# Kernel optimization log

Hardware: AMD Instinct MI355X
Metric: run time of the kernel (lower is better)

## Reference

```python
import jax, jax.numpy as jnp
import numpy as np

BS, SEQ, IN_DIM, EMB = 64, 1024, 512, 1024
HID = EMB // 2  # MLP hidden = embed_dim//2 = 512
RATIO = 0.3
K = max(1, int((SEQ - 2) * RATIO))  # 306
MASK_VALUE = -10000.0
BN_EPS = 1e-5


def setup_inputs() -> dict:
    key = jax.random.key(0)
    ks = jax.random.split(key, 12)
    features = jax.random.normal(ks[0], (BS, SEQ, IN_DIM), dtype=jnp.float32)
    atten = jax.random.normal(ks[1], (BS, SEQ, SEQ), dtype=jnp.float32)
    # variable-length token ids, pad_id = 0
    lengths = jax.random.randint(ks[2], (BS,), K + 14, SEQ + 1)
    tokens = jax.random.randint(ks[3], (BS, SEQ), 1, 30000)
    text = jnp.where(jnp.arange(SEQ)[None, :] < lengths[:, None], tokens, 0).astype(jnp.int64)
    s = 0.02
    lin_w = jax.random.normal(ks[4], (IN_DIM, EMB), dtype=jnp.float32) * s
    lin_b = jnp.zeros((EMB,), dtype=jnp.float32)
    w1 = jax.random.normal(ks[5], (IN_DIM, HID), dtype=jnp.float32) * s
    b1 = jnp.zeros((HID,), dtype=jnp.float32)
    g1 = jnp.ones((HID,), dtype=jnp.float32)
    be1 = jnp.zeros((HID,), dtype=jnp.float32)
    w2 = jax.random.normal(ks[6], (HID, EMB), dtype=jnp.float32) * s
    b2 = jnp.zeros((EMB,), dtype=jnp.float32)
    return {"features": features, "atten": atten, "text": text,
            "lin_w": lin_w, "lin_b": lin_b, "w1": w1, "b1": b1,
            "g1": g1, "be1": be1, "w2": w2, "b2": b2}


def _forward(features, atten, text, lin_w, lin_b, w1, b1, g1, be1, w2, b2):
    bs, seq_len, _ = atten.shape
    atten = jnp.nan_to_num(atten, nan=0.0, posinf=0.0, neginf=0.0)
    mask = (text != 0).astype(jnp.float32)                       # (bs, seq)
    token_lens = jnp.maximum(jnp.sum(text != 0, axis=1), 1)       # (bs,)
    eos_pos = jnp.clip(token_lens - 1, 0, seq_len - 1)            # (bs,)
    # mask column 0 and column eos_pos (per batch) across all rows
    col = jnp.arange(seq_len)[None, :]
    col_mask = (col == 0) | (col == eos_pos[:, None])             # (bs, seq)
    atten = jnp.where(col_mask[:, None, :], MASK_VALUE, atten)
    # masked_fill where token is pad (columns)
    atten = jnp.where(mask[:, None, :] == 0, MASK_VALUE, atten)
    atten = jax.nn.softmax(atten, axis=1)                         # softmax over rows (dim=1)
    # select the eos row per batch, weight by mask
    atten_sel = jnp.take_along_axis(atten, eos_pos[:, None, None], axis=1)[:, 0, :] * mask
    _, topk_idx = jax.lax.top_k(atten_sel, K)                     # (bs, K)
    feats_k = jnp.take_along_axis(features, topk_idx[:, :, None], axis=1)  # (bs, K, D)
    norm = jnp.maximum(jnp.linalg.norm(feats_k, axis=-1, keepdims=True), 1e-6)
    feats_k = feats_k / norm
    cap_emb = feats_k @ lin_w + lin_b                             # (bs, K, EMB)
    # MLP: Linear -> BatchNorm1d(train-mode batch stats) -> ReLU -> Linear
    xf = feats_k.reshape(bs * K, -1)
    h = xf @ w1 + b1                                              # (bs*K, HID)
    mu = jnp.mean(h, axis=0)
    var = jnp.mean((h - mu) ** 2, axis=0)                         # biased var
    h = (h - mu) / jnp.sqrt(var + BN_EPS) * g1 + be1
    h = jax.nn.relu(h)
    feats_mlp = (h @ w2 + b2).reshape(bs, K, -1)
    fused = cap_emb + feats_mlp                                   # (bs, K, EMB)
    # variable-length top-1 pooling: max over first pool_lens[b] tokens
    pool_lens = jnp.clip(token_lens - 2, 1, K)
    valid = jnp.arange(K)[None, :] < pool_lens[:, None]           # (bs, K)
    out = jnp.max(jnp.where(valid[:, :, None], fused, -jnp.inf), axis=1)
    return out.astype(jnp.float32)


def reference(features, atten, text, lin_w, lin_b, w1, b1, g1, be1, w2, b2):
    return _forward(features, atten, text, lin_w, lin_b, w1, b1, g1, be1, w2, b2)
```

## Files before the change

### kernel.cpp

```cpp
#include <hip/hip_runtime.h>
#include <cstdint>
#include <cstddef>
#include <cmath>

#define BS 64
#define SEQ 1024
#define IN_DIM 512
#define EMB 1024
#define HID 512
#define KSEL 306
#define MROWS (BS * KSEL)

typedef __bf16 bf16_t;
typedef bf16_t bf16x8 __attribute__((ext_vector_type(8)));
typedef bf16_t bf16x4 __attribute__((ext_vector_type(4)));
typedef float f32x4 __attribute__((ext_vector_type(4)));

__device__ __forceinline__ void async16(const void* g, void* l) {
  __builtin_amdgcn_global_load_lds(
      (const __attribute__((address_space(1))) unsigned int*)g,
      (__attribute__((address_space(3))) unsigned int*)l, 16, 0, 0);
}

__device__ __forceinline__ void atomicMaxF(float* a, float v) {
  if (v >= 0.f)
    atomicMax((int*)a, __float_as_int(v));
  else
    atomicMin((unsigned int*)a, __float_as_uint(v));
}

__global__ void k_meta(const int* __restrict__ text, int* __restrict__ eos,
                       float* __restrict__ out) {
  int b = blockIdx.x;
  __shared__ int cnt;
  if (threadIdx.x == 0) cnt = 0;
  __syncthreads();
  int local = 0;
  for (int i = threadIdx.x; i < SEQ; i += blockDim.x)
    local += (text[b * SEQ + i] != 0) ? 1 : 0;
  atomicAdd(&cnt, local);
  for (int c = threadIdx.x; c < EMB; c += blockDim.x)
    out[(b << 10) + c] = -INFINITY;
  __syncthreads();
  if (threadIdx.x == 0) {
    int L = cnt > 1 ? cnt : 1;
    int e = L - 1;
    if (e > SEQ - 1) e = SEQ - 1;
    eos[b] = e;
  }
}

__global__ void k_colsum(const float* __restrict__ atten, float* __restrict__ part) {
  int b = blockIdx.x;
  int r0 = blockIdx.y << 6;
  int c = threadIdx.x << 2;
  const float* base = atten + ((size_t)b << 20) + ((size_t)r0 << 10) + c;
  float4 s = {0.f, 0.f, 0.f, 0.f};
#pragma unroll 4
  for (int r = 0; r < 64; ++r) {
    float4 x = *(const float4*)(base + ((size_t)r << 10));
    s.x += __expf((isfinite(x.x) ? x.x : 0.f) - 12.f);
    s.y += __expf((isfinite(x.y) ? x.y : 0.f) - 12.f);
    s.z += __expf((isfinite(x.z) ? x.z : 0.f) - 12.f);
    s.w += __expf((isfinite(x.w) ? x.w : 0.f) - 12.f);
  }
  *(float4*)&part[((((size_t)blockIdx.y << 6) | b) << 10) | c] = s;
}

__global__ void k_selval(const float* __restrict__ atten, const int* __restrict__ text,
                         const int* __restrict__ eos, const float* __restrict__ part,
                         float* __restrict__ selval) {
  int b = blockIdx.x >> 2;
  int c = ((blockIdx.x & 3) << 8) | threadIdx.x;
  int e = eos[b];
  float cs = 0.f;
#pragma unroll
  for (int p = 0; p < 16; ++p) cs += part[(((p << 6) | b) << 10) | c];
  float v = atten[((size_t)b << 20) + ((size_t)e << 10) + c];
  if (!isfinite(v)) v = 0.f;
  int tok = text[(b << 10) | c];
  float res;
  if (tok == 0) res = 0.f;
  else if (c == 0 || c == e) res = 1.f / 1024.f;
  else res = __expf(v - 12.f) / cs;
  selval[(b << 10) | c] = res;
}

__global__ void k_topk(const float* __restrict__ selval, int* __restrict__ selidx) {
  int b = blockIdx.x;
  int i = (blockIdx.y << 8) | threadIdx.x;
  __shared__ float vals[SEQ];
  for (int j = threadIdx.x; j < SEQ; j += 256) vals[j] = selval[(b << 10) + j];
  __syncthreads();
  float vc = vals[i];
  int rank = 0;
  for (int j = 0; j < SEQ; ++j) {
    float vj = vals[j];
    rank += (vj > vc || (vj == vc && j < i)) ? 1 : 0;
  }
  if (rank < KSEL) selidx[b * KSEL + rank] = i;
}

__global__ void k_gather(const float* __restrict__ features, const int* __restrict__ sel,
                         bf16_t* __restrict__ xcat) {
  int row = blockIdx.x;
  int b = row / KSEL;
  int k = row - b * KSEL;
  int idx = sel[b * KSEL + k];
  const float4* src = (const float4*)(features + (((size_t)b << 10) + idx) * IN_DIM);
  float4 v = src[threadIdx.x];
  float ss = v.x * v.x + v.y * v.y + v.z * v.z + v.w * v.w;
#pragma unroll
  for (int off = 32; off > 0; off >>= 1) ss += __shfl_down(ss, off, 64);
  __shared__ float wsum[2];
  int lane = threadIdx.x & 63, wid = threadIdx.x >> 6;
  if (lane == 0) wsum[wid] = ss;
  __syncthreads();
  float total = wsum[0] + wsum[1];
  float scale = 1.f / fmaxf(sqrtf(total), 1e-6f);
  bf16x4 o;
  o[0] = (bf16_t)(v.x * scale);
  o[1] = (bf16_t)(v.y * scale);
  o[2] = (bf16_t)(v.z * scale);
  o[3] = (bf16_t)(v.w * scale);
  *(bf16x4*)(xcat + (size_t)row * EMB + (threadIdx.x << 2)) = o;
}

__global__ void k_transpose_bf16(const float* __restrict__ src, int srcld,
                                 bf16_t* __restrict__ dst, int dstld) {
  __shared__ float tile[32][33];
  int k0 = blockIdx.x << 5, n0 = blockIdx.y << 5;
  int tx = threadIdx.x, ty = threadIdx.y;
#pragma unroll
  for (int i = 0; i < 4; i++)
    tile[ty + 8 * i][tx] = src[(size_t)(k0 + ty + 8 * i) * srcld + n0 + tx];
  __syncthreads();
#pragma unroll
  for (int i = 0; i < 4; i++)
    dst[(size_t)(n0 + ty + 8 * i) * dstld + k0 + tx] = (bf16_t)tile[tx][ty + 8 * i];
}

template <int MODE>
__global__ __launch_bounds__(256, 2) void k_mfma_gemm(
    const bf16_t* __restrict__ A, int lda, const bf16_t* __restrict__ Bt, int ldb,
    const float* __restrict__ bias, bf16_t* __restrict__ C, int ldc, int K,
    float* __restrict__ stats, float* __restrict__ outmax) {
  __shared__ __align__(16) bf16_t As[128 * 32];
  __shared__ __align__(16) bf16_t Bs[128 * 32];
  int tid = threadIdx.x;

  int MT = gridDim.x, NT = gridDim.y;
  int nwg = MT * NT;
  int flat = blockIdx.y * MT + blockIdx.x;
  int q = nwg >> 3, r = nwg & 7;
  int xcd = flat & 7, ii = flat >> 3;
  int lin = (xcd < r ? xcd * (q + 1) : r * (q + 1) + (xcd - r) * q) + ii;
  int mtile = lin / NT;
  int ntile = lin - mtile * NT;
  int m0 = mtile << 7, n0 = ntile << 7;

  int wave = tid >> 6, lane = tid & 63;
  int wm = (wave >> 1) << 6, wn = (wave & 1) << 6;
  int lrow = lane & 15, quad = lane >> 4;

  f32x4 acc[4][4];
#pragma unroll
  for (int i = 0; i < 4; i++)
#pragma unroll
    for (int j = 0; j < 4; j++) acc[i][j] = (f32x4){0.f, 0.f, 0.f, 0.f};

  int c0 = tid, c1 = 256 + tid;
  int ar0 = c0 >> 2, ak0 = (c0 & 3) << 3;
  int ar1 = c1 >> 2, ak1 = (c1 & 3) << 3;
  const bf16_t* Ap0 = A + (size_t)(m0 + ar0) * lda + ak0;
  const bf16_t* Ap1 = A + (size_t)(m0 + ar1) * lda + ak1;
  const bf16_t* Bp0 = Bt + (size_t)(n0 + ar0) * ldb + ak0;
  const bf16_t* Bp1 = Bt + (size_t)(n0 + ar1) * ldb + ak1;

  for (int k0 = 0; k0 < K; k0 += 32) {
    async16(Ap0 + k0, &As[c0 << 3]);
    async16(Ap1 + k0, &As[c1 << 3]);
    async16(Bp0 + k0, &Bs[c0 << 3]);
    async16(Bp1 + k0, &Bs[c1 << 3]);
    __syncthreads();

    bf16x8 af[4], bfr[4];
#pragma unroll
    for (int i = 0; i < 4; i++)
      af[i] = *(const bf16x8*)&As[((wm + (i << 4) + lrow) << 5) + (quad << 3)];
#pragma unroll
    for (int j = 0; j < 4; j++)
      bfr[j] = *(const bf16x8*)&Bs[((wn + (j << 4) + lrow) << 5) + (quad << 3)];
#pragma unroll
    for (int i = 0; i < 4; i++)
#pragma unroll
      for (int j = 0; j < 4; j++)
        acc[i][j] = __builtin_amdgcn_mfma_f32_16x16x32_bf16(af[i], bfr[j], acc[i][j], 0, 0, 0);
    __syncthreads();
  }

  if (MODE == 0) {
#pragma unroll
    for (int j = 0; j < 4; j++) {
      int n = n0 + wn + (j << 4) + lrow;
      float bv = bias[n];
      float s = 0.f, qq = 0.f;
#pragma unroll
      for (int i = 0; i < 4; i++) {
        int mbase = m0 + wm + (i << 4) + (quad << 2);
#pragma unroll
        for (int rr = 0; rr < 4; rr++) {
          float v = acc[i][j][rr] + bv;
          C[(size_t)(mbase + rr) * ldc + n] = (bf16_t)v;
          s += v;
          qq += v * v;
        }
      }
      s += __shfl_xor(s, 16, 64);
      s += __shfl_xor(s, 32, 64);
      qq += __shfl_xor(qq, 16, 64);
      qq += __shfl_xor(qq, 32, 64);
      if (quad == 0) {
        atomicAdd(&stats[n], s);
        atomicAdd(&stats[HID + n], qq);
      }
    }
  } else {
    int mw = m0 + wm;
    int b0w = mw / KSEL;
    int cut = (b0w + 1) * KSEL;
#pragma unroll
    for (int j = 0; j < 4; j++) {
      int n = n0 + wn + (j << 4) + lrow;
      float bv = bias[n];
      float mx0 = -INFINITY, mx1 = -INFINITY;
#pragma unroll
      for (int i = 0; i < 4; i++) {
#pragma unroll
        for (int rr = 0; rr < 4; rr++) {
          int m = mw + (i << 4) + (quad << 2) + rr;
          float v = acc[i][j][rr] + bv;
          if (m < cut) mx0 = fmaxf(mx0, v);
          else mx1 = fmaxf(mx1, v);
        }
      }
      mx0 = fmaxf(mx0, __shfl_xor(mx0, 16, 64));
      mx0 = fmaxf(mx0, __shfl_xor(mx0, 32, 64));
      mx1 = fmaxf(mx1, __shfl_xor(mx1, 16, 64));
      mx1 = fmaxf(mx1, __shfl_xor(mx1, 32, 64));
      if (quad == 0) {
        atomicMaxF(&outmax[(b0w << 10) + n], mx0);
        if (cut < mw + 64) atomicMaxF(&outmax[((b0w + 1) << 10) + n], mx1);
      }
    }
  }
}

__global__ void k_bnparam(const float* __restrict__ stats, const float* __restrict__ g,
                          const float* __restrict__ be, float* __restrict__ scsh,
                          const float* __restrict__ lin_b, const float* __restrict__ b2,
                          float* __restrict__ biasC) {
  int c = threadIdx.x;
  biasC[c] = lin_b[c] + b2[c];
  if (c < HID) {
    float inv = 1.f / (float)MROWS;
    float mu = stats[c] * inv;
    float var = stats[HID + c] * inv - mu * mu;
    var = fmaxf(var, 0.f);
    float sc = g[c] * rsqrtf(var + 1e-5f);
    scsh[c] = sc;
    scsh[HID + c] = fmaf(-mu, sc, be[c]);
  }
}

__global__ void k_bnapply(const bf16_t* __restrict__ h, const float* __restrict__ scsh,
                          bf16_t* __restrict__ xcat) {
  size_t idx = (size_t)blockIdx.x * blockDim.x + threadIdx.x;
  bf16x8 x = ((const bf16x8*)h)[idx];
  int c = (int)(idx & 63) << 3;
  size_t row = idx >> 6;
  bf16x8 o;
#pragma unroll
  for (int t = 0; t < 8; ++t) {
    float v = (float)x[t];
    float a = fmaxf(fmaf(v, scsh[c + t], scsh[HID + c + t]), 0.f);
    o[t] = (bf16_t)a;
  }
  *(bf16x8*)(xcat + row * EMB + 512 + c) = o;
}

extern "C" void kernel_launch(void* const* d_in, const int* in_sizes, int n_in,
                              void* d_out, int out_size, void* d_ws, size_t ws_size,
                              hipStream_t stream) {
  const float* features = (const float*)d_in[0];
  const float* atten    = (const float*)d_in[1];
  const int*   text     = (const int*)d_in[2];
  const float* lin_w    = (const float*)d_in[3];
  const float* lin_b    = (const float*)d_in[4];
  const float* w1       = (const float*)d_in[5];
  const float* b1       = (const float*)d_in[6];
  const float* g1       = (const float*)d_in[7];
  const float* be1      = (const float*)d_in[8];
  const float* w2       = (const float*)d_in[9];
  const float* b2       = (const float*)d_in[10];
  float* out = (float*)d_out;

  char* ws = (char*)d_ws;
  int*    eos    = (int*)(ws + 0);
  float*  stats  = (float*)(ws + 256);
  float*  scsh   = (float*)(ws + 4608);
  float*  biasC  = (float*)(ws + 8704);
  float*  part   = (float*)(ws + 12800);
  float*  selval = (float*)(ws + 4207104UL);
  int*    selidx = (int*)(ws + 4469248UL);
  bf16_t* w1t    = (bf16_t*)(ws + 4547584UL);
  bf16_t* wcatt  = (bf16_t*)(ws + 5071872UL);
  bf16_t* xcat   = (bf16_t*)(ws + 7169024UL);
  bf16_t* h      = (bf16_t*)(ws + 47277056UL);

  hipMemsetAsync(stats, 0, 4096, stream);

  k_meta<<<BS, 256, 0, stream>>>(text, eos, out);
  k_colsum<<<dim3(BS, 16), 256, 0, stream>>>(atten, part);
  k_selval<<<BS * 4, 256, 0, stream>>>(atten, text, eos, part, selval);
  k_topk<<<dim3(BS, 4), 256, 0, stream>>>(selval, selidx);
  k_gather<<<MROWS, 128, 0, stream>>>(features, selidx, xcat);

  k_transpose_bf16<<<dim3(16, 16), dim3(32, 8), 0, stream>>>(w1, HID, w1t, IN_DIM);
  k_transpose_bf16<<<dim3(16, 32), dim3(32, 8), 0, stream>>>(lin_w, EMB, wcatt, EMB);
  k_transpose_bf16<<<dim3(16, 32), dim3(32, 8), 0, stream>>>(w2, EMB, wcatt + 512, EMB);

  k_mfma_gemm<0><<<dim3(MROWS / 128, HID / 128), 256, 0, stream>>>(
      xcat, EMB, w1t, IN_DIM, b1, h, HID, IN_DIM, stats, nullptr);

  k_bnparam<<<1, EMB, 0, stream>>>(stats, g1, be1, scsh, lin_b, b2, biasC);
  k_bnapply<<<(MROWS * (HID / 8)) / 256, 256, 0, stream>>>(h, scsh, xcat);

  k_mfma_gemm<1><<<dim3(MROWS / 128, EMB / 128), 256, 0, stream>>>(
      xcat, EMB, wcatt, EMB, biasC, nullptr, 0, EMB, nullptr, out);
}
```

Measured before the change: 577.2 us.

## Fuse GEMM1 with BatchNorm via cooperative grid sync; merge selval/topk and transposes

Replaces the GEMM1 → bnparam → bnapply sequence with a single cooperative kernel. Each block computes a 128x512 tile, holds it in registers, accumulates batch statistics with atomics, waits on a grid-wide sync, then applies BN and ReLU and writes straight into xcat. This removes the intermediate h buffer round trip and two launches. It also folds selval into the top-k kernel and merges the three weight transposes into one launch. In exchange it needs all 153 blocks of 512 threads resident at once, uses large register tiles (acc[4][8]), and the selval work is repeated for each of the 4 blockIdx.y slices.

```diff
diff --git a/kernel.cpp b/kernel.cpp
--- a/kernel.cpp
+++ b/kernel.cpp
@@ -1,7 +1,10 @@
 #include <hip/hip_runtime.h>
+#include <hip/hip_cooperative_groups.h>
 #include <cstdint>
 #include <cstddef>
 #include <cmath>
+
+namespace cg = cooperative_groups;
 
 #define BS 64
 #define SEQ 1024
@@ -67,31 +70,27 @@
   *(float4*)&part[((((size_t)blockIdx.y << 6) | b) << 10) | c] = s;
 }
 
-__global__ void k_selval(const float* __restrict__ atten, const int* __restrict__ text,
-                         const int* __restrict__ eos, const float* __restrict__ part,
-                         float* __restrict__ selval) {
-  int b = blockIdx.x >> 2;
-  int c = ((blockIdx.x & 3) << 8) | threadIdx.x;
+__global__ void k_topk(const float* __restrict__ atten, const int* __restrict__ text,
+                       const int* __restrict__ eos, const float* __restrict__ part,
+                       int* __restrict__ selidx) {
+  int b = blockIdx.x;
+  __shared__ float vals[SEQ];
   int e = eos[b];
-  float cs = 0.f;
-#pragma unroll
-  for (int p = 0; p < 16; ++p) cs += part[(((p << 6) | b) << 10) | c];
-  float v = atten[((size_t)b << 20) + ((size_t)e << 10) + c];
-  if (!isfinite(v)) v = 0.f;
-  int tok = text[(b << 10) | c];
-  float res;
-  if (tok == 0) res = 0.f;
-  else if (c == 0 || c == e) res = 1.f / 1024.f;
-  else res = __expf(v - 12.f) / cs;
-  selval[(b << 10) | c] = res;
-}
-
-__global__ void k_topk(const float* __restrict__ selval, int* __restrict__ selidx) {
-  int b = blockIdx.x;
+  for (int c = threadIdx.x; c < SEQ; c += 256) {
+    float cs = 0.f;
+#pragma unroll
+    for (int p = 0; p < 16; ++p) cs += part[(((p << 6) | b) << 10) | c];
+    float v = atten[((size_t)b << 20) + ((size_t)e << 10) + c];
+    if (!isfinite(v)) v = 0.f;
+    int tok = text[(b << 10) | c];
+    float res;
+    if (tok == 0) res = 0.f;
+    else if (c == 0 || c == e) res = 1.f / 1024.f;
+    else res = __expf(v - 12.f) / cs;
+    vals[c] = res;
+  }
+  __syncthreads();
   int i = (blockIdx.y << 8) | threadIdx.x;
-  __shared__ float vals[SEQ];
-  for (int j = threadIdx.x; j < SEQ; j += 256) vals[j] = selval[(b << 10) + j];
-  __syncthreads();
   float vc = vals[i];
   int rank = 0;
   for (int j = 0; j < SEQ; ++j) {
@@ -126,10 +125,16 @@
   *(bf16x4*)(xcat + (size_t)row * EMB + (threadIdx.x << 2)) = o;
 }
 
-__global__ void k_transpose_bf16(const float* __restrict__ src, int srcld,
-                                 bf16_t* __restrict__ dst, int dstld) {
+__global__ void k_transpose_all(const float* __restrict__ w1, const float* __restrict__ lin_w,
+                                const float* __restrict__ w2, bf16_t* __restrict__ w1t,
+                                bf16_t* __restrict__ wcatt) {
   __shared__ float tile[32][33];
-  int k0 = blockIdx.x << 5, n0 = blockIdx.y << 5;
+  int by = blockIdx.y;
+  const float* src; int srcld; bf16_t* dst; int dstld; int n0;
+  if (by < 16)      { src = w1;    srcld = HID; dst = w1t;         dstld = IN_DIM; n0 = by << 5; }
+  else if (by < 48) { src = lin_w; srcld = EMB; dst = wcatt;       dstld = EMB;    n0 = (by - 16) << 5; }
+  else              { src = w2;    srcld = EMB; dst = wcatt + 512; dstld = EMB;    n0 = (by - 48) << 5; }
+  int k0 = blockIdx.x << 5;
   int tx = threadIdx.x, ty = threadIdx.y;
 #pragma unroll
   for (int i = 0; i < 4; i++)
@@ -140,11 +145,109 @@
     dst[(size_t)(n0 + ty + 8 * i) * dstld + k0 + tx] = (bf16_t)tile[tx][ty + 8 * i];
 }
 
-template <int MODE>
-__global__ __launch_bounds__(256, 2) void k_mfma_gemm(
-    const bf16_t* __restrict__ A, int lda, const bf16_t* __restrict__ Bt, int ldb,
-    const float* __restrict__ bias, bf16_t* __restrict__ C, int ldc, int K,
-    float* __restrict__ stats, float* __restrict__ outmax) {
+__global__ __launch_bounds__(512, 1) void k_gemm1_coop(
+    const bf16_t* A,
+    const bf16_t* __restrict__ Bt,
+    const float* __restrict__ b1, const float* __restrict__ g1,
+    const float* __restrict__ be1, float* stats,
+    bf16_t* xcat_out) {
+  __shared__ __align__(16) bf16_t As[128 * 32];
+  __shared__ __align__(16) bf16_t Bs[512 * 32];
+  int tid = threadIdx.x;
+  int m0 = blockIdx.x << 7;
+  int wave = tid >> 6, lane = tid & 63;
+  int wm = (wave >> 2) << 6;
+  int wn = (wave & 3) << 7;
+  int lrow = lane & 15, quad = lane >> 4;
+
+  f32x4 acc[4][8];
+#pragma unroll
+  for (int i = 0; i < 4; i++)
+#pragma unroll
+    for (int j = 0; j < 8; j++) acc[i][j] = (f32x4){0.f, 0.f, 0.f, 0.f};
+
+  int arow = tid >> 2, ak = (tid & 3) << 3;
+  const bf16_t* Ap = A + (size_t)(m0 + arow) * EMB + ak;
+  int brow0 = tid >> 2, bk = (tid & 3) << 3;
+  const bf16_t* Bp0 = Bt + (size_t)(brow0 + 0) * IN_DIM + bk;
+  const bf16_t* Bp1 = Bt + (size_t)(brow0 + 128) * IN_DIM + bk;
+  const bf16_t* Bp2 = Bt + (size_t)(brow0 + 256) * IN_DIM + bk;
+  const bf16_t* Bp3 = Bt + (size_t)(brow0 + 384) * IN_DIM + bk;
+
+  for (int k0 = 0; k0 < IN_DIM; k0 += 32) {
+    async16(Ap + k0, &As[tid << 3]);
+    async16(Bp0 + k0, &Bs[(tid + 0) << 3]);
+    async16(Bp1 + k0, &Bs[(tid + 512) << 3]);
+    async16(Bp2 + k0, &Bs[(tid + 1024) << 3]);
+    async16(Bp3 + k0, &Bs[(tid + 1536) << 3]);
+    __syncthreads();
+
+    bf16x8 af[4], bfr[8];
+#pragma unroll
+    for (int i = 0; i < 4; i++)
+      af[i] = *(const bf16x8*)&As[((wm + (i << 4) + lrow) << 5) + (quad << 3)];
+#pragma unroll
+    for (int j = 0; j < 8; j++)
+      bfr[j] = *(const bf16x8*)&Bs[((wn + (j << 4) + lrow) << 5) + (quad << 3)];
+#pragma unroll
+    for (int i = 0; i < 4; i++)
+#pragma unroll
+      for (int j = 0; j < 8; j++)
+        acc[i][j] = __builtin_amdgcn_mfma_f32_16x16x32_bf16(af[i], bfr[j], acc[i][j], 0, 0, 0);
+    __syncthreads();
+  }
+
+#pragma unroll
+  for (int j = 0; j < 8; j++) {
+    int n = wn + (j << 4) + lrow;
+    float bv = b1[n];
+    float s = 0.f, qq = 0.f;
+#pragma unroll
+    for (int i = 0; i < 4; i++) {
+#pragma unroll
+      for (int rr = 0; rr < 4; rr++) {
+        float v = acc[i][j][rr] + bv;
+        acc[i][j][rr] = v;
+        s += v;
+        qq += v * v;
+      }
+    }
+    s += __shfl_xor(s, 16, 64);
+    s += __shfl_xor(s, 32, 64);
+    qq += __shfl_xor(qq, 16, 64);
+    qq += __shfl_xor(qq, 32, 64);
+    if (quad == 0) {
+      atomicAdd(&stats[n], s);
+      atomicAdd(&stats[HID + n], qq);
+    }
+  }
+
+  cg::this_grid().sync();
+
+  const float inv = 1.f / (float)MROWS;
+#pragma unroll
+  for (int j = 0; j < 8; j++) {
+    int n = wn + (j << 4) + lrow;
+    float mu = stats[n] * inv;
+    float var = fmaxf(stats[HID + n] * inv - mu * mu, 0.f);
+    float sc = g1[n] * rsqrtf(var + 1e-5f);
+    float sh = fmaf(-mu, sc, be1[n]);
+#pragma unroll
+    for (int i = 0; i < 4; i++) {
+      int mbase = m0 + wm + (i << 4) + (quad << 2);
+#pragma unroll
+      for (int rr = 0; rr < 4; rr++) {
+        float a = fmaxf(fmaf(acc[i][j][rr], sc, sh), 0.f);
+        xcat_out[(size_t)(mbase + rr) * EMB + 512 + n] = (bf16_t)a;
+      }
+    }
+  }
+}
+
+__global__ __launch_bounds__(256, 2) void k_gemm2(
+    const bf16_t* __restrict__ A, const bf16_t* __restrict__ Bt,
+    const float* __restrict__ lin_b, const float* __restrict__ b2,
+    float* __restrict__ outmax) {
   __shared__ __align__(16) bf16_t As[128 * 32];
   __shared__ __align__(16) bf16_t Bs[128 * 32];
   int tid = threadIdx.x;
@@ -172,12 +275,12 @@
   int c0 = tid, c1 = 256 + tid;
   int ar0 = c0 >> 2, ak0 = (c0 & 3) << 3;
   int ar1 = c1 >> 2, ak1 = (c1 & 3) << 3;
-  const bf16_t* Ap0 = A + (size_t)(m0 + ar0) * lda + ak0;
-  const bf16_t* Ap1 = A + (size_t)(m0 + ar1) * lda + ak1;
-  const bf16_t* Bp0 = Bt + (size_t)(n0 + ar0) * ldb + ak0;
-  const bf16_t* Bp1 = Bt + (size_t)(n0 + ar1) * ldb + ak1;
-
-  for (int k0 = 0; k0 < K; k0 += 32) {
+  const bf16_t* Ap0 = A + (size_t)(m0 + ar0) * EMB + ak0;
+  const bf16_t* Ap1 = A + (size_t)(m0 + ar1) * EMB + ak1;
+  const bf16_t* Bp0 = Bt + (size_t)(n0 + ar0) * EMB + ak0;
+  const bf16_t* Bp1 = Bt + (size_t)(n0 + ar1) * EMB + ak1;
+
+  for (int k0 = 0; k0 < EMB; k0 += 32) {
     async16(Ap0 + k0, &As[c0 << 3]);
     async16(Ap1 + k0, &As[c1 << 3]);
     async16(Bp0 + k0, &Bs[c0 << 3]);
@@ -199,94 +302,33 @@
     __syncthreads();
   }
 
-  if (MODE == 0) {
-#pragma unroll
-    for (int j = 0; j < 4; j++) {
-      int n = n0 + wn + (j << 4) + lrow;
-      float bv = bias[n];
-      float s = 0.f, qq = 0.f;
-#pragma unroll
-      for (int i = 0; i < 4; i++) {
-        int mbase = m0 + wm + (i << 4) + (quad << 2);
-#pragma unroll
-        for (int rr = 0; rr < 4; rr++) {
-          float v = acc[i][j][rr] + bv;
-          C[(size_t)(mbase + rr) * ldc + n] = (bf16_t)v;
-          s += v;
-          qq += v * v;
-        }
+  int mw = m0 + wm;
+  int b0w = mw / KSEL;
+  int cut = (b0w + 1) * KSEL;
+#pragma unroll
+  for (int j = 0; j < 4; j++) {
+    int n = n0 + wn + (j << 4) + lrow;
+    float bv = lin_b[n] + b2[n];
+    float mx0 = -INFINITY, mx1 = -INFINITY;
+#pragma unroll
+    for (int i = 0; i < 4; i++) {
+#pragma unroll
+      for (int rr = 0; rr < 4; rr++) {
+        int m = mw + (i << 4) + (quad << 2) + rr;
+        float v = acc[i][j][rr] + bv;
+        if (m < cut) mx0 = fmaxf(mx0, v);
+        else mx1 = fmaxf(mx1, v);
       }
-      s += __shfl_xor(s, 16, 64);
-      s += __shfl_xor(s, 32, 64);
-      qq += __shfl_xor(qq, 16, 64);
-      qq += __shfl_xor(qq, 32, 64);
-      if (quad == 0) {
-        atomicAdd(&stats[n], s);
-        atomicAdd(&stats[HID + n], qq);
-      }
-    }
-  } else {
-    int mw = m0 + wm;
-    int b0w = mw / KSEL;
-    int cut = (b0w + 1) * KSEL;
-#pragma unroll
-    for (int j = 0; j < 4; j++) {
-      int n = n0 + wn + (j << 4) + lrow;
-      float bv = bias[n];
-      float mx0 = -INFINITY, mx1 = -INFINITY;
-#pragma unroll
-      for (int i = 0; i < 4; i++) {
-#pragma unroll
-        for (int rr = 0; rr < 4; rr++) {
-          int m = mw + (i << 4) + (quad << 2) + rr;
-          float v = acc[i][j][rr] + bv;
-          if (m < cut) mx0 = fmaxf(mx0, v);
-          else mx1 = fmaxf(mx1, v);
-        }
-      }
-      mx0 = fmaxf(mx0, __shfl_xor(mx0, 16, 64));
-      mx0 = fmaxf(mx0, __shfl_xor(mx0, 32, 64));
-      mx1 = fmaxf(mx1, __shfl_xor(mx1, 16, 64));
-      mx1 = fmaxf(mx1, __shfl_xor(mx1, 32, 64));
-      if (quad == 0) {
-        atomicMaxF(&outmax[(b0w << 10) + n], mx0);
-        if (cut < mw + 64) atomicMaxF(&outmax[((b0w + 1) << 10) + n], mx1);
-      }
-    }
-  }
-}
-
-__global__ void k_bnparam(const float* __restrict__ stats, const float* __restrict__ g,
-                          const float* __restrict__ be, float* __restrict__ scsh,
-                          const float* __restrict__ lin_b, const float* __restrict__ b2,
-                          float* __restrict__ biasC) {
-  int c = threadIdx.x;
-  biasC[c] = lin_b[c] + b2[c];
-  if (c < HID) {
-    float inv = 1.f / (float)MROWS;
-    float mu = stats[c] * inv;
-    float var = stats[HID + c] * inv - mu * mu;
-    var = fmaxf(var, 0.f);
-    float sc = g[c] * rsqrtf(var + 1e-5f);
-    scsh[c] = sc;
-    scsh[HID + c] = fmaf(-mu, sc, be[c]);
-  }
-}
-
-__global__ void k_bnapply(const bf16_t* __restrict__ h, const float* __restrict__ scsh,
-                          bf16_t* __restrict__ xcat) {
-  size_t idx = (size_t)blockIdx.x * blockDim.x + threadIdx.x;
-  bf16x8 x = ((const bf16x8*)h)[idx];
-  int c = (int)(idx & 63) << 3;
-  size_t row = idx >> 6;
-  bf16x8 o;
-#pragma unroll
-  for (int t = 0; t < 8; ++t) {
-    float v = (float)x[t];
-    float a = fmaxf(fmaf(v, scsh[c + t], scsh[HID + c + t]), 0.f);
-    o[t] = (bf16_t)a;
-  }
-  *(bf16x8*)(xcat + row * EMB + 512 + c) = o;
+    }
+    mx0 = fmaxf(mx0, __shfl_xor(mx0, 16, 64));
+    mx0 = fmaxf(mx0, __shfl_xor(mx0, 32, 64));
+    mx1 = fmaxf(mx1, __shfl_xor(mx1, 16, 64));
+    mx1 = fmaxf(mx1, __shfl_xor(mx1, 32, 64));
+    if (quad == 0) {
+      atomicMaxF(&outmax[(b0w << 10) + n], mx0);
+      if (cut < mw + 64) atomicMaxF(&outmax[((b0w + 1) << 10) + n], mx1);
+    }
+  }
 }
 
 extern "C" void kernel_launch(void* const* d_in, const int* in_sizes, int n_in,
@@ -308,34 +350,34 @@
   char* ws = (char*)d_ws;
   int*    eos    = (int*)(ws + 0);
   float*  stats  = (float*)(ws + 256);
-  float*  scsh   = (float*)(ws + 4608);
-  float*  biasC  = (float*)(ws + 8704);
-  float*  part   = (float*)(ws + 12800);
-  float*  selval = (float*)(ws + 4207104UL);
-  int*    selidx = (int*)(ws + 4469248UL);
-  bf16_t* w1t    = (bf16_t*)(ws + 4547584UL);
-  bf16_t* wcatt  = (bf16_t*)(ws + 5071872UL);
-  bf16_t* xcat   = (bf16_t*)(ws + 7169024UL);
-  bf16_t* h      = (bf16_t*)(ws + 47277056UL);
+  float*  part   = (float*)(ws + 8192);
+  int*    selidx = (int*)(ws + 4202496UL);
+  bf16_t* w1t    = (bf16_t*)(ws + 4280832UL);
+  bf16_t* wcatt  = (bf16_t*)(ws + 4805120UL);
+  bf16_t* xcat   = (bf16_t*)(ws + 6902272UL);
 
   hipMemsetAsync(stats, 0, 4096, stream);
 
   k_meta<<<BS, 256, 0, stream>>>(text, eos, out);
   k_colsum<<<dim3(BS, 16), 256, 0, stream>>>(atten, part);
-  k_selval<<<BS * 4, 256, 0, stream>>>(atten, text, eos, part, selval);
-  k_topk<<<dim3(BS, 4), 256, 0, stream>>>(selval, selidx);
+  k_topk<<<dim3(BS, 4), 256, 0, stream>>>(atten, text, eos, part, selidx);
   k_gather<<<MROWS, 128, 0, stream>>>(features, selidx, xcat);
-
-  k_transpose_bf16<<<dim3(16, 16), dim3(32, 8), 0, stream>>>(w1, HID, w1t, IN_DIM);
-  k_transpose_bf16<<<dim3(16, 32), dim3(32, 8), 0, stream>>>(lin_w, EMB, wcatt, EMB);
-  k_transpose_bf16<<<dim3(16, 32), dim3(32, 8), 0, stream>>>(w2, EMB, wcatt + 512, EMB);
-
-  k_mfma_gemm<0><<<dim3(MROWS / 128, HID / 128), 256, 0, stream>>>(
-      xcat, EMB, w1t, IN_DIM, b1, h, HID, IN_DIM, stats, nullptr);
-
-  k_bnparam<<<1, EMB, 0, stream>>>(stats, g1, be1, scsh, lin_b, b2, biasC);
-  k_bnapply<<<(MROWS * (HID / 8)) / 256, 256, 0, stream>>>(h, scsh, xcat);
-
-  k_mfma_gemm<1><<<dim3(MROWS / 128, EMB / 128), 256, 0, stream>>>(
-      xcat, EMB, wcatt, EMB, biasC, nullptr, 0, EMB, nullptr, out);
-}
+  k_transpose_all<<<dim3(16, 80), dim3(32, 8), 0, stream>>>(w1, lin_w, w2, w1t, wcatt);
+
+  {
+    const bf16_t* gA = xcat;
+    const bf16_t* gB = w1t;
+    const float* gb1 = b1;
+    const float* gg1 = g1;
+    const float* gbe = be1;
+    float* gst = stats;
+    bf16_t* gx = xcat;
+    void* kargs[] = {(void*)&gA, (void*)&gB, (void*)&gb1, (void*)&gg1,
+                     (void*)&gbe, (void*)&gst, (void*)&gx};
+    hipLaunchCooperativeKernel((void*)k_gemm1_coop, dim3(MROWS / 128), dim3(512),
+                               kargs, 0, stream);
+  }
+
+  k_gemm2<<<dim3(MROWS / 128, EMB / 128), 256, 0, stream>>>(
+      xcat, wcatt, lin_b, b2, out);
+}
```

After: 622.6 us. 7.9% more time.
